# Performance work log

Measured on AMD Instinct MI355X. Metric: run time of the kernel, lower is better.

Reference implementation:

```python
import jax, jax.numpy as jnp
import numpy as np
from jax import lax

K = 5          # CARAFE kernel size
STRIDE = 2     # scale_factor (downsample)
ENC_PAD = 1    # (encoder_kernel-1)*dilation/2 = 1


def conv2d(x, w, b, stride, padding):
    out = lax.conv_general_dilated(
        x, w, (stride, stride), [(padding, padding), (padding, padding)],
        dimension_numbers=('NCHW', 'OIHW', 'NCHW'))
    return out + b[None, :, None, None]


def setup_inputs() -> dict:
    key = jax.random.key(0)
    ks = jax.random.split(key, 4)
    B, C, H, W = 4, 256, 128, 128
    CC = 64
    x = jax.random.normal(ks[0], (B, C, H, W), dtype=jnp.float32)
    w_comp = jax.random.normal(ks[1], (CC, C, 1, 1), dtype=jnp.float32) * (1.0 / np.sqrt(C))
    b_comp = jnp.zeros((CC,), jnp.float32)
    w_enc = jax.random.normal(ks[2], (K * K, CC, 3, 3), dtype=jnp.float32) * (1.0 / np.sqrt(CC * 9))
    b_enc = jnp.zeros((K * K,), jnp.float32)
    w_kenc = jax.random.normal(ks[3], (16, CC, 3, 3), dtype=jnp.float32) * (1.0 / np.sqrt(CC * 9))
    b_kenc = jnp.zeros((16,), jnp.float32)
    return {'x': x, 'w_comp': w_comp, 'b_comp': b_comp,
            'w_enc': w_enc, 'b_enc': b_enc,
            'w_kenc': w_kenc, 'b_kenc': b_kenc}


def reference(x, w_comp, b_comp, w_enc, b_enc, w_kenc, b_kenc):
    B, C, H, W = x.shape
    # channel compressor (1x1 conv)
    cx = conv2d(x, w_comp, b_comp, stride=1, padding=0)          # (B,CC,H,W)
    # content encoder -> mask logits at downsampled grid
    mask = conv2d(cx, w_enc, b_enc, stride=STRIDE, padding=ENC_PAD)   # (B,K*K,Ho,Wo)
    # kernel encoder -> per-pixel temperature via channel product (Power/PI)
    ke = conv2d(cx, w_kenc, b_kenc, stride=STRIDE, padding=ENC_PAD)   # (B,16,Ho,Wo)
    i = jnp.clip(jnp.prod(ke, axis=1, keepdims=True), -10.0, 10.0)    # (B,1,Ho,Wo)
    mask = mask * i
    Ho, Wo = mask.shape[2], mask.shape[3]
    # softmax over the K*K kernel positions (group=1)
    mask = jax.nn.softmax(mask.reshape(B, 1, K * K, Ho, Wo), axis=2)
    mask = mask.reshape(B, K * K, Ho, Wo)
    # feature reassembly: unfold + weighted sum over kernel window
    pad = K // 2
    patches = lax.conv_general_dilated_patches(
        x, filter_shape=(K, K), window_strides=(STRIDE, STRIDE),
        padding=[(pad, pad), (pad, pad)],
        dimension_numbers=('NCHW', 'OIHW', 'NCHW'))                   # (B, C*K*K, Ho, Wo)
    patches = patches.reshape(B, C, K * K, Ho, Wo)
    out = jnp.einsum('bckhw,bkhw->bchw', patches, mask)
    return out
```

## Files before the change

### kernel.cpp

```cpp
#include <hip/hip_runtime.h>

#define H_IN   128
#define W_IN   128
#define HW_IN  16384
#define C_IN   256
#define CC     64
#define HO     64
#define WO     64
#define HWO    4096
#define NB     4
#define NPX    16384
#define NCHP   48

#define OFF_WC    0
#define OFF_WE    16384
#define OFF_CX    44032
#define OFF_PART  4238336
#define OFF_MASK  5811200

__global__ __launch_bounds__(256) void prep_kernel(
    const float* __restrict__ wc, const float* __restrict__ we,
    const float* __restrict__ wk, float* __restrict__ ws) {
  int i = blockIdx.x * 256 + threadIdx.x;
  if (i < 16384) {
    int ccg = i >> 11, c = (i >> 3) & 255, j = i & 7;
    ws[OFF_WC + i] = wc[(ccg * 8 + j) * C_IN + c];
  } else if (i < 44032) {
    int e = i - 16384;
    int chg = e / 3456, r = e - chg * 3456;
    int row = r / 6, j = r - row * 6;
    int ch = chg * 6 + j;
    float v = 0.f;
    if (ch < 25)      v = we[ch * 576 + row];
    else if (ch < 41) v = wk[(ch - 25) * 576 + row];
    ws[OFF_WE + e] = v;
  }
}

__global__ __launch_bounds__(1024) void compress_kernel(
    const float* __restrict__ x, const float* __restrict__ bcomp,
    const float* __restrict__ wsr, float* __restrict__ cx) {
  __shared__ float red[8][64][33];
  int tid = threadIdx.x;
  int wv = tid >> 6, lane = tid & 63;
  int ccg = __builtin_amdgcn_readfirstlane(wv & 7);
  int kh  = __builtin_amdgcn_readfirstlane(wv >> 3);
  int gq = blockIdx.x * 64 + lane;
  int b = gq >> 12;
  int p = (gq & 4095) << 2;
  const float* xb = x + (size_t)b * C_IN * HW_IN + p;
  const float* wp = wsr + OFF_WC + ccg * (256 * 8);
  float4 acc[8];
#pragma unroll
  for (int j = 0; j < 8; ++j) acc[j] = make_float4(0.f, 0.f, 0.f, 0.f);
  int cbase = kh * 128;
  float4 xv[4], xn[4];
#pragma unroll
  for (int u = 0; u < 4; ++u)
    xv[u] = *(const float4*)(xb + (size_t)(cbase + u) * HW_IN);
  for (int c0 = 0; c0 < 128; c0 += 4) {
    if (c0 + 4 < 128) {
#pragma unroll
      for (int u = 0; u < 4; ++u)
        xn[u] = *(const float4*)(xb + (size_t)(cbase + c0 + 4 + u) * HW_IN);
    }
#pragma unroll
    for (int u = 0; u < 4; ++u) {
      const float* wrow = wp + (cbase + c0 + u) * 8;
      float4 xu = xv[u];
#pragma unroll
      for (int j = 0; j < 8; ++j) {
        float wj = wrow[j];
        acc[j].x = fmaf(wj, xu.x, acc[j].x);
        acc[j].y = fmaf(wj, xu.y, acc[j].y);
        acc[j].z = fmaf(wj, xu.z, acc[j].z);
        acc[j].w = fmaf(wj, xu.w, acc[j].w);
      }
    }
#pragma unroll
    for (int u = 0; u < 4; ++u) xv[u] = xn[u];
  }
  if (kh == 1) {
    float* d = &red[ccg][lane][0];
#pragma unroll
    for (int j = 0; j < 8; ++j) {
      d[j * 4 + 0] = acc[j].x; d[j * 4 + 1] = acc[j].y;
      d[j * 4 + 2] = acc[j].z; d[j * 4 + 3] = acc[j].w;
    }
  }
  __syncthreads();
  if (kh == 0) {
    const float* d = &red[ccg][lane][0];
#pragma unroll
    for (int j = 0; j < 8; ++j) {
      int cc = ccg * 8 + j;
      float bj = bcomp[cc];
      float4 o;
      o.x = acc[j].x + d[j * 4 + 0] + bj;
      o.y = acc[j].y + d[j * 4 + 1] + bj;
      o.z = acc[j].z + d[j * 4 + 2] + bj;
      o.w = acc[j].w + d[j * 4 + 3] + bj;
      *(float4*)(cx + ((size_t)b * CC + cc) * HW_IN + p) = o;
    }
  }
}

__global__ __launch_bounds__(1024) void encoder_kernel(
    const float* __restrict__ wsr, float* __restrict__ part) {
  const float* cxall = wsr + OFF_CX;
  int tid = threadIdx.x;
  int wv = tid >> 6, lane = tid & 63;
  int chg = __builtin_amdgcn_readfirstlane(wv & 7);
  int kh  = __builtin_amdgcn_readfirstlane(wv >> 3);
  int px = blockIdx.x * 64 + lane;
  int b = px >> 12, pix = px & 4095;
  int ho = pix >> 6, wo = pix & 63;
  const float* cxb = cxall + (size_t)b * CC * HW_IN;
  const float* wbase = wsr + OFF_WE + chg * (576 * 6);
  float acc[6];
#pragma unroll
  for (int j = 0; j < 6; ++j) acc[j] = 0.f;
  for (int ci = kh * 32; ci < kh * 32 + 32; ++ci) {
    const float* base = cxb + (size_t)ci * HW_IN;
#pragma unroll
    for (int k3 = 0; k3 < 3; ++k3) {
      int hi = 2 * ho - 1 + k3;
      if ((unsigned)hi < 128u) {
#pragma unroll
        for (int kw = 0; kw < 3; ++kw) {
          int wi = 2 * wo - 1 + kw;
          int wic = wi < 0 ? 0 : (wi > 127 ? 127 : wi);
          float v = base[hi * W_IN + wic];
          v = ((unsigned)wi < 128u) ? v : 0.f;
          const float* w = wbase + (ci * 9 + k3 * 3 + kw) * 6;
#pragma unroll
          for (int j = 0; j < 6; ++j) acc[j] = fmaf(w[j], v, acc[j]);
        }
      }
    }
  }
  float* pb = part + (size_t)kh * NCHP * NPX + px;
#pragma unroll
  for (int j = 0; j < 6; ++j) pb[(size_t)(chg * 6 + j) * NPX] = acc[j];
}

__global__ __launch_bounds__(64) void softmax_kernel(
    const float* __restrict__ wsr, const float* __restrict__ benc,
    const float* __restrict__ bkenc, float* __restrict__ mask) {
  const float* part = wsr + OFF_PART;
  int px = blockIdx.x * 64 + threadIdx.x;
  float lg[41];
#pragma unroll
  for (int ch = 0; ch < 41; ++ch) {
    float s = (ch < 25) ? benc[ch] : bkenc[ch - 25];
    s += part[(size_t)ch * NPX + px];
    s += part[(size_t)(NCHP + ch) * NPX + px];
    lg[ch] = s;
  }
  float prod = lg[25];
#pragma unroll
  for (int ch = 26; ch < 41; ++ch) prod *= lg[ch];
  float iv = fminf(fmaxf(prod, -10.f), 10.f);
  float m = -1e30f;
#pragma unroll
  for (int ch = 0; ch < 25; ++ch) { lg[ch] *= iv; m = fmaxf(m, lg[ch]); }
  float sum = 0.f;
#pragma unroll
  for (int ch = 0; ch < 25; ++ch) { lg[ch] = __expf(lg[ch] - m); sum += lg[ch]; }
  float inv = 1.0f / sum;
#pragma unroll
  for (int ch = 0; ch < 25; ++ch)
    mask[(size_t)ch * NPX + px] = lg[ch] * inv;
}

__global__ __launch_bounds__(256) void reassemble_kernel(
    const float* __restrict__ x, const float* __restrict__ wsr,
    float* __restrict__ out) {
  __shared__ float lds[4][11][136];
  const float* mask = wsr + OFF_MASK;
  int tid = threadIdx.x;
  int gb = blockIdx.x;
  int cg = gb & 63, hog = (gb >> 6) & 15, b = gb >> 10;
  int hi0 = hog * 8 - 2;

  for (int i = tid; i < 352; i += 256) {
    int ch = i / 88; int r = i - ch * 88; int row = r >> 3; int p = r & 7;
    int idx = (p < 4) ? p : (128 + p);
    lds[ch][row][idx] = 0.f;
  }
  for (int i = tid; i < 1408; i += 256) {
    int ch = i / 352; int r = i - ch * 352;
    int row = r >> 5, c4 = r & 31;
    int hi = hi0 + row;
    float4 v = make_float4(0.f, 0.f, 0.f, 0.f);
    if ((unsigned)hi < 128u) {
      int c = cg * 4 + ch;
      v = *(const float4*)(x + ((size_t)(b * C_IN + c) * HW_IN) + hi * W_IN + c4 * 4);
    }
    *(float4*)(&lds[ch][row][4 + c4 * 4]) = v;
  }
  __syncthreads();

  int wo = tid & 63, hs = tid >> 6;
  int ho = hog * 4 + hs;
  int opix = ho * WO + wo;
  int gpx = b * HWO + opix;
  float mk[25];
#pragma unroll
  for (int k = 0; k < 25; ++k)
    mk[k] = mask[(size_t)k * NPX + gpx];
#pragma unroll
  for (int ch = 0; ch < 4; ++ch) {
    const float* lp = &lds[ch][2 * hs][2 + 2 * wo];
    float s = 0.f;
#pragma unroll
    for (int kh = 0; kh < 5; ++kh)
#pragma unroll
      for (int kw = 0; kw < 5; ++kw)
        s = fmaf(mk[kh * 5 + kw], lp[kh * 136 + kw], s);
    int c = cg * 4 + ch;
    out[(size_t)(b * C_IN + c) * HWO + opix] = s;
  }
}

extern "C" void kernel_launch(void* const* d_in, const int* in_sizes, int n_in,
                              void* d_out, int out_size, void* d_ws, size_t ws_size,
                              hipStream_t stream) {
  const float* x      = (const float*)d_in[0];
  const float* w_comp = (const float*)d_in[1];
  const float* b_comp = (const float*)d_in[2];
  const float* w_enc  = (const float*)d_in[3];
  const float* b_enc  = (const float*)d_in[4];
  const float* w_kenc = (const float*)d_in[5];
  const float* b_kenc = (const float*)d_in[6];
  float* ws  = (float*)d_ws;
  float* out = (float*)d_out;

  prep_kernel<<<172, 256, 0, stream>>>(w_comp, w_enc, w_kenc, ws);
  compress_kernel<<<256, 1024, 0, stream>>>(x, b_comp, ws, ws + OFF_CX);
  encoder_kernel<<<256, 1024, 0, stream>>>(ws, ws + OFF_PART);
  softmax_kernel<<<256, 64, 0, stream>>>(ws, b_enc, b_kenc, ws + OFF_MASK);
  reassemble_kernel<<<4096, 256, 0, stream>>>(x, ws, out);
}
```

Before: 195.6 us.

## Tile encoder conv through LDS with all output channels per thread

The encoder now stages 8-input-channel slabs of the compressed feature map (with halo rows and zero padding) in shared memory. Each thread computes all 41 mask and kernel-encoder channels for one output pixel, so every input value is loaded once and reused across channels. Input channels are split into 8 partial sums that the softmax kernel adds up. The weight layout is reordered to a dense 48-wide row per tap, and the workspace offset grows to hold the larger partial buffer. The cost is 41 accumulators per thread, which raises register pressure, plus 4x more partial-sum traffic between the two kernels.

```diff
diff --git a/kernel.cpp b/kernel.cpp
--- a/kernel.cpp
+++ b/kernel.cpp
@@ -16,7 +16,7 @@
 #define OFF_WE    16384
 #define OFF_CX    44032
 #define OFF_PART  4238336
-#define OFF_MASK  5811200
+#define OFF_MASK  10529792
 
 __global__ __launch_bounds__(256) void prep_kernel(
     const float* __restrict__ wc, const float* __restrict__ we,
@@ -27,9 +27,7 @@
     ws[OFF_WC + i] = wc[(ccg * 8 + j) * C_IN + c];
   } else if (i < 44032) {
     int e = i - 16384;
-    int chg = e / 3456, r = e - chg * 3456;
-    int row = r / 6, j = r - row * 6;
-    int ch = chg * 6 + j;
+    int row = e / 48, ch = e - row * 48;
     float v = 0.f;
     if (ch < 25)      v = we[ch * 576 + row];
     else if (ch < 41) v = wk[(ch - 25) * 576 + row];
@@ -105,43 +103,54 @@
   }
 }
 
-__global__ __launch_bounds__(1024) void encoder_kernel(
+__global__ __launch_bounds__(256) void encoder_kernel(
     const float* __restrict__ wsr, float* __restrict__ part) {
-  const float* cxall = wsr + OFF_CX;
+  __shared__ float lds[8][9][136];
+  const float* cx   = wsr + OFF_CX;
+  const float* wall = wsr + OFF_WE;
+  int gb = blockIdx.x;
+  int hog = gb & 15, b = (gb >> 4) & 3, ph = gb >> 6;
   int tid = threadIdx.x;
-  int wv = tid >> 6, lane = tid & 63;
-  int chg = __builtin_amdgcn_readfirstlane(wv & 7);
-  int kh  = __builtin_amdgcn_readfirstlane(wv >> 3);
-  int px = blockIdx.x * 64 + lane;
-  int b = px >> 12, pix = px & 4095;
-  int ho = pix >> 6, wo = pix & 63;
-  const float* cxb = cxall + (size_t)b * CC * HW_IN;
-  const float* wbase = wsr + OFF_WE + chg * (576 * 6);
-  float acc[6];
-#pragma unroll
-  for (int j = 0; j < 6; ++j) acc[j] = 0.f;
-  for (int ci = kh * 32; ci < kh * 32 + 32; ++ci) {
-    const float* base = cxb + (size_t)ci * HW_IN;
+  int ci0 = ph * 8;
+  int hi0 = hog * 8 - 1;
+
+  for (int i = tid; i < 288; i += 256) {
+    int ci = i / 36; int r = (i % 36) >> 2; int j = i & 3;
+    lds[ci][r][j] = 0.f;
+  }
+  for (int i = tid; i < 2304; i += 256) {
+    int ci = i / 288; int r2 = i - ci * 288;
+    int row = r2 >> 5, c4 = r2 & 31;
+    int hi = hi0 + row;
+    float4 v = make_float4(0.f, 0.f, 0.f, 0.f);
+    if ((unsigned)hi < 128u)
+      v = *(const float4*)(cx + ((size_t)(b * CC + ci0 + ci) * HW_IN) + hi * W_IN + c4 * 4);
+    *(float4*)(&lds[ci][row][4 + c4 * 4]) = v;
+  }
+  __syncthreads();
+
+  int wo = tid & 63, hs = tid >> 6;
+  float acc[41];
+#pragma unroll
+  for (int ch = 0; ch < 41; ++ch) acc[ch] = 0.f;
+  const float* lp = &lds[0][2 * hs][3 + 2 * wo];
+#pragma unroll
+  for (int ci = 0; ci < 8; ++ci) {
 #pragma unroll
     for (int k3 = 0; k3 < 3; ++k3) {
-      int hi = 2 * ho - 1 + k3;
-      if ((unsigned)hi < 128u) {
-#pragma unroll
-        for (int kw = 0; kw < 3; ++kw) {
-          int wi = 2 * wo - 1 + kw;
-          int wic = wi < 0 ? 0 : (wi > 127 ? 127 : wi);
-          float v = base[hi * W_IN + wic];
-          v = ((unsigned)wi < 128u) ? v : 0.f;
-          const float* w = wbase + (ci * 9 + k3 * 3 + kw) * 6;
-#pragma unroll
-          for (int j = 0; j < 6; ++j) acc[j] = fmaf(w[j], v, acc[j]);
-        }
+#pragma unroll
+      for (int kw = 0; kw < 3; ++kw) {
+        float v = lp[ci * 1224 + k3 * 136 + kw];
+        const float* w = wall + ((ci0 + ci) * 9 + k3 * 3 + kw) * 48;
+#pragma unroll
+        for (int ch = 0; ch < 41; ++ch) acc[ch] = fmaf(w[ch], v, acc[ch]);
       }
     }
   }
-  float* pb = part + (size_t)kh * NCHP * NPX + px;
-#pragma unroll
-  for (int j = 0; j < 6; ++j) pb[(size_t)(chg * 6 + j) * NPX] = acc[j];
+  int px = b * HWO + (hog * 4 + hs) * 64 + wo;
+  float* pb = part + (size_t)ph * NCHP * NPX + px;
+#pragma unroll
+  for (int ch = 0; ch < 41; ++ch) pb[(size_t)ch * NPX] = acc[ch];
 }
 
 __global__ __launch_bounds__(64) void softmax_kernel(
@@ -153,8 +162,9 @@
 #pragma unroll
   for (int ch = 0; ch < 41; ++ch) {
     float s = (ch < 25) ? benc[ch] : bkenc[ch - 25];
-    s += part[(size_t)ch * NPX + px];
-    s += part[(size_t)(NCHP + ch) * NPX + px];
+#pragma unroll
+    for (int q = 0; q < 8; ++q)
+      s += part[(size_t)(q * NCHP + ch) * NPX + px];
     lg[ch] = s;
   }
   float prod = lg[25];
@@ -238,7 +248,7 @@
 
   prep_kernel<<<172, 256, 0, stream>>>(w_comp, w_enc, w_kenc, ws);
   compress_kernel<<<256, 1024, 0, stream>>>(x, b_comp, ws, ws + OFF_CX);
-  encoder_kernel<<<256, 1024, 0, stream>>>(ws, ws + OFF_PART);
+  encoder_kernel<<<512, 256, 0, stream>>>(ws, ws + OFF_PART);
   softmax_kernel<<<256, 64, 0, stream>>>(ws, b_enc, b_kenc, ws + OFF_MASK);
   reassemble_kernel<<<4096, 256, 0, stream>>>(x, ws, out);
 }
```

New measurement: 270.0 us. +38.0%, slower.
